# Kernel tuning notes

Measured on AMD Instinct MI355X. Metric: run time of the kernel, lower is better.

The kernel has to match this reference:

```python
import jax, jax.numpy as jnp
import numpy as np

N = 100000
E = 3200000
IN_DIM, HID, MLP_HID, K = 3, 64, 128, 15


def setup_inputs() -> dict:
    key = jax.random.key(0)
    ks = jax.random.split(key, 10)
    x = jax.random.normal(ks[0], (N, IN_DIM), dtype=jnp.float32)
    edge_index = jax.random.randint(ks[1], (2, E), 0, N, dtype=jnp.int32)
    def glorot(k, shape):
        lim = float(np.sqrt(6.0 / (shape[0] + shape[1])))
        return jax.random.uniform(k, shape, jnp.float32, -lim, lim)
    return {
        "x": x,
        "edge_index": edge_index,
        "W1": glorot(ks[2], (IN_DIM, HID)), "b1": jnp.zeros((HID,), jnp.float32),
        "W2": glorot(ks[3], (HID, HID)),    "b2": jnp.zeros((HID,), jnp.float32),
        "Wm1": glorot(ks[4], (HID, MLP_HID)), "bm1": jnp.zeros((MLP_HID,), jnp.float32),
        "Wm2": glorot(ks[5], (MLP_HID, K)),   "bm2": jnp.zeros((K,), jnp.float32),
    }


def _gcn_layer(h, W, b, src, dst, deg_inv_sqrt, n):
    # h: [N, Fin] -> [N, Fout]; GCNConv: D^-1/2 (A+I) D^-1/2 (h W) + b
    hw = h @ W  # dense GEMM first (Fin small)
    norm = deg_inv_sqrt[src] * deg_inv_sqrt[dst]  # [E+N]
    msg = hw[src] * norm[:, None]                 # irregular gather, [E+N, Fout]
    out = jax.ops.segment_sum(msg, dst, num_segments=n)  # scatter-add
    return out + b


def reference(x, edge_index, W1, b1, W2, b2, Wm1, bm1, Wm2, bm2):
    n = x.shape[0]
    loops = jnp.arange(n, dtype=edge_index.dtype)
    src = jnp.concatenate([edge_index[0], loops])  # self-loops appended
    dst = jnp.concatenate([edge_index[1], loops])
    deg = jax.ops.segment_sum(jnp.ones_like(dst, dtype=x.dtype), dst, num_segments=n)
    deg_inv_sqrt = jnp.where(deg > 0, jax.lax.rsqrt(jnp.maximum(deg, 1.0)), 0.0)

    h = jax.nn.elu(_gcn_layer(x, W1, b1, src, dst, deg_inv_sqrt, n))
    h = jax.nn.elu(_gcn_layer(h, W2, b2, src, dst, deg_inv_sqrt, n))
    # MLP (dropout is identity in eval mode)
    h = jax.nn.elu(h @ Wm1 + bm1)
    H = h @ Wm2 + bm2
    return jax.nn.softmax(H, axis=1)  # [N, K]
```

## Files before the change

kernel.cpp:

```cpp
#include <hip/hip_runtime.h>
#include <hip/hip_fp16.h>
#include <math.h>


#define SPAN 128
#define CAP  4608
#define CH   8192
#define EPT  32
#define H2P  88
#define MSP2 136

typedef _Float16 v8hf __attribute__((ext_vector_type(8)));
typedef float    v4f  __attribute__((ext_vector_type(4)));

__device__ __forceinline__ float elu(float v) { return v > 0.f ? v : expm1f(v); }

__global__ __launch_bounds__(256) void prep_kernel(const float* __restrict__ W2,
    const float* __restrict__ Wm1, __half* __restrict__ W2t, __half* __restrict__ Wm1t,
    int* __restrict__ cursor, int NBK) {
    int tid = blockIdx.x * 256 + threadIdx.x;
    if (tid < NBK) cursor[tid] = 0;
    if (tid < 64 * 64) {
        int f = tid >> 6, k = tid & 63;
        W2t[f * 64 + k] = __float2half(W2[k * 64 + f]);
    }
    if (tid < 128 * 64) {
        int j = tid >> 6, f = tid & 63;
        Wm1t[j * 64 + f] = __float2half(Wm1[f * 128 + j]);
    }
}

__global__ __launch_bounds__(256) void scatter_kernel(const int* __restrict__ src,
    const int* __restrict__ dst, int* __restrict__ cursor, unsigned* __restrict__ colb,
    int E, int NBK) {
    __shared__ int hist[1024];
    __shared__ unsigned gb[1024];
    int tid = threadIdx.x;
    int chunk = blockIdx.x;
    for (int i = tid; i < NBK; i += 256) hist[i] = 0;
    __syncthreads();
    int base = chunk * CH;
    int cnt = min(CH, E - base);
    unsigned br[EPT], dt[EPT];
#pragma unroll
    for (int j = 0; j < EPT; ++j) {
        int idx = j * 256 + tid;
        br[j] = 0xFFFFFFFFu;
        if (idx < cnt) {
            int e = base + idx;
            int s = src[e], d = dst[e];
            int b = d >> 7;
            int r = atomicAdd(&hist[b], 1);
            br[j] = ((unsigned)b << 13) | (unsigned)r;
            dt[j] = ((unsigned)(d & 127) << 17) | (unsigned)s;
        }
    }
    __syncthreads();
    for (int b = tid; b < NBK; b += 256) {
        int c = hist[b];
        gb[b] = (unsigned)(b * CAP) + (c ? (unsigned)atomicAdd(&cursor[b], c) : 0u);
    }
    __syncthreads();
#pragma unroll
    for (int j = 0; j < EPT; ++j) {
        if (br[j] != 0xFFFFFFFFu) {
            int b = br[j] >> 13;
            int r = br[j] & 8191;
            unsigned pos = gb[b] + (unsigned)r;
            if (pos < (unsigned)(b + 1) * CAP) colb[pos] = dt[j];
        }
    }
}

__global__ __launch_bounds__(256) void csr_sort_kernel(const unsigned* __restrict__ colb,
    const int* __restrict__ cursor, const float* __restrict__ x,
    int* __restrict__ row_ptr, int* __restrict__ col,
    float* __restrict__ dis, __half* __restrict__ sxh, int N, int NBK) {
    __shared__ unsigned ebuf[CAP];
    __shared__ int sbuf[CAP];
    __shared__ int cnt[SPAN], pref[SPAN], fill[SPAN];
    __shared__ int redbuf[256];
    int b = blockIdx.x, tid = threadIdx.x;
    int n = min(cursor[b], CAP);
    int base = b * CAP;
    int partial = 0;
    for (int i2 = tid; i2 < b; i2 += 256) partial += min(cursor[i2], CAP);
    redbuf[tid] = partial;
    if (tid < SPAN) cnt[tid] = 0;
    for (int i = tid; i < n; i += 256) ebuf[i] = colb[base + i];
    __syncthreads();
    for (int off = 128; off; off >>= 1) {
        if (tid < off) redbuf[tid] += redbuf[tid + off];
        __syncthreads();
    }
    int bb = redbuf[0];
    for (int i = tid; i < n; i += 256) atomicAdd(&cnt[(ebuf[i] >> 17) & 127], 1);
    __syncthreads();
    if (tid < SPAN) pref[tid] = cnt[tid];
    __syncthreads();
    for (int off = 1; off < SPAN; off <<= 1) {
        int xv = (tid < SPAN && tid >= off) ? pref[tid - off] : 0;
        __syncthreads();
        if (tid < SPAN) pref[tid] += xv;
        __syncthreads();
    }
    if (tid < SPAN) {
        int ex = pref[tid] - cnt[tid];
        fill[tid] = ex;
        int node = b * SPAN + tid;
        if (node < N) {
            row_ptr[node] = bb + ex;
            float r = rsqrtf((float)(cnt[tid] + 1));
            dis[node] = r;
            __half2 h0 = __floats2half2_rn(r * x[node * 3 + 0], r * x[node * 3 + 1]);
            __half2 h1 = __floats2half2_rn(r * x[node * 3 + 2], 0.f);
            uint2 w; w.x = *(unsigned*)&h0; w.y = *(unsigned*)&h1;
            *(uint2*)(sxh + (size_t)node * 4) = w;
        }
    }
    if (b == NBK - 1 && tid == 0) row_ptr[N] = bb + n;
    __syncthreads();
    for (int i = tid; i < n; i += 256) {
        unsigned e = ebuf[i];
        int pos = atomicAdd(&fill[(e >> 17) & 127], 1);
        sbuf[pos] = (int)(e & 0x1FFFF);
    }
    __syncthreads();
    for (int i = tid; i < n; i += 256) col[bb + i] = sbuf[i];
}

__global__ void agg3_kernel(const __half* __restrict__ sxh, const int* __restrict__ row_ptr,
                            const int* __restrict__ col, const float* __restrict__ dis,
                            const float* __restrict__ W1, const float* __restrict__ b1,
                            __half* __restrict__ s1h, int N) {
    int wave = (blockIdx.x * blockDim.x + threadIdx.x) >> 6;
    int lane = threadIdx.x & 63;
    if (wave >= N) return;
    int d = wave;
    int start = row_ptr[d], end = row_ptr[d + 1];
    float a0 = 0.f, a1 = 0.f, a2v = 0.f;
    for (int i = start + lane; i < end; i += 64) {
        uint2 rq = *(const uint2*)(sxh + (size_t)col[i] * 4);
        float2 u0 = __half22float2(*(__half2*)&rq.x);
        float2 u1 = __half22float2(*(__half2*)&rq.y);
        a0 += u0.x; a1 += u0.y; a2v += u1.x;
    }
#pragma unroll
    for (int off = 32; off; off >>= 1) {
        a0  += __shfl_xor(a0, off);
        a1  += __shfl_xor(a1, off);
        a2v += __shfl_xor(a2v, off);
    }
    {
        uint2 rq = *(const uint2*)(sxh + (size_t)d * 4);
        float2 u0 = __half22float2(*(__half2*)&rq.x);
        float2 u1 = __half22float2(*(__half2*)&rq.y);
        a0 += u0.x; a1 += u0.y; a2v += u1.x;
    }
    float r = dis[d];
    float v = r * (a0 * W1[lane] + a1 * W1[64 + lane] + a2v * W1[128 + lane]) + b1[lane];
    s1h[(size_t)d * 64 + lane] = __float2half(r * elu(v));
}

__global__ void agg64_kernel(const __half2* __restrict__ s1h, const int* __restrict__ row_ptr,
                             const int* __restrict__ col, const float* __restrict__ dis,
                             __half2* __restrict__ a2h, int N) {
    int wave = (blockIdx.x * blockDim.x + threadIdx.x) >> 6;
    int lane = threadIdx.x & 63;
    int hl = lane & 31;
    int d = wave * 2 + (lane >> 5);
    bool act = d < N;
    int start = 0, end = 0;
    if (act) { start = row_ptr[d]; end = row_ptr[d + 1]; }
    float a0x = 0.f, a0y = 0.f, a1x = 0.f, a1y = 0.f;
    float a2x = 0.f, a2y = 0.f, a3x = 0.f, a3y = 0.f;
    float a4x = 0.f, a4y = 0.f, a5x = 0.f, a5y = 0.f;
    float a6x = 0.f, a6y = 0.f, a7x = 0.f, a7y = 0.f;
    if (act) {
        float2 v = __half22float2(s1h[(size_t)d * 32 + hl]);
        a0x = v.x; a0y = v.y;
    }
    int i = start;
    for (; i + 7 < end; i += 8) {
        int c0 = col[i],     c1 = col[i + 1], c2 = col[i + 2], c3 = col[i + 3];
        int c4 = col[i + 4], c5 = col[i + 5], c6 = col[i + 6], c7 = col[i + 7];
        float2 v0 = __half22float2(s1h[(size_t)c0 * 32 + hl]);
        float2 v1 = __half22float2(s1h[(size_t)c1 * 32 + hl]);
        float2 v2 = __half22float2(s1h[(size_t)c2 * 32 + hl]);
        float2 v3 = __half22float2(s1h[(size_t)c3 * 32 + hl]);
        float2 v4 = __half22float2(s1h[(size_t)c4 * 32 + hl]);
        float2 v5 = __half22float2(s1h[(size_t)c5 * 32 + hl]);
        float2 v6 = __half22float2(s1h[(size_t)c6 * 32 + hl]);
        float2 v7 = __half22float2(s1h[(size_t)c7 * 32 + hl]);
        a0x += v0.x; a0y += v0.y; a1x += v1.x; a1y += v1.y;
        a2x += v2.x; a2y += v2.y; a3x += v3.x; a3y += v3.y;
        a4x += v4.x; a4y += v4.y; a5x += v5.x; a5y += v5.y;
        a6x += v6.x; a6y += v6.y; a7x += v7.x; a7y += v7.y;
    }
    for (; i < end; ++i) {
        float2 v = __half22float2(s1h[(size_t)col[i] * 32 + hl]);
        a0x += v.x; a0y += v.y;
    }
    if (act) {
        float r = dis[d];
        float ox = r * (((a0x + a1x) + (a2x + a3x)) + ((a4x + a5x) + (a6x + a7x)));
        float oy = r * (((a0y + a1y) + (a2y + a3y)) + ((a4y + a5y) + (a6y + a7y)));
        a2h[(size_t)d * 32 + hl] = __floats2half2_rn(ox, oy);
    }
}

__global__ __launch_bounds__(256) void h1_kernel(const __half* __restrict__ a2h,
    const __half* __restrict__ W2t, const float* __restrict__ b2g,
    const __half* __restrict__ Wm1t, const float* __restrict__ bm1g,
    const float* __restrict__ Wm2g, const float* __restrict__ bm2g,
    float* __restrict__ out, int N) {
    __shared__ __align__(16) __half h2s[64 * H2P];
    __shared__ __align__(16) __half ms[64 * MSP2];
    __shared__ float Wt2[128 * 16];
    __shared__ float b2s[64], bm1s[128], bm2s[16];
    int tid = threadIdx.x;
    if (tid < 64)  b2s[tid]  = b2g[tid];
    if (tid < 128) bm1s[tid] = bm1g[tid];
    if (tid < 16)  bm2s[tid] = (tid < 15) ? bm2g[tid] : 0.f;
    for (int i = tid; i < 128 * 16; i += 256) {
        int j = i >> 4, c = i & 15;
        Wt2[i] = (c < 15) ? Wm2g[j * 15 + c] : 0.f;
    }
    __syncthreads();

    int wave = tid >> 6, lane = tid & 63;
    int q = lane >> 4, l16 = lane & 15;
    int base = blockIdx.x * 64;

    {
        int nodeRow = base + wave * 16 + l16;
        size_t arow = (size_t)min(nodeRow, N - 1) * 64;
        v8hf af0 = *(const v8hf*)(a2h + arow + q * 8);
        v8hf af1 = *(const v8hf*)(a2h + arow + 32 + q * 8);
#pragma unroll
        for (int fb = 0; fb < 4; ++fb) {
            float bb = b2s[fb * 16 + l16];
            v4f acc = {bb, bb, bb, bb};
            v8hf b0 = *(const v8hf*)(W2t + (fb * 16 + l16) * 64 + q * 8);
            v8hf b1 = *(const v8hf*)(W2t + (fb * 16 + l16) * 64 + 32 + q * 8);
            acc = __builtin_amdgcn_mfma_f32_16x16x32_f16(af0, b0, acc, 0, 0, 0);
            acc = __builtin_amdgcn_mfma_f32_16x16x32_f16(af1, b1, acc, 0, 0, 0);
#pragma unroll
            for (int r = 0; r < 4; ++r)
                h2s[(wave * 16 + q * 4 + r) * H2P + fb * 16 + l16] =
                    __float2half(elu(acc[r]));
        }
    }
    __syncthreads();
    {
        int arow = (wave * 16 + l16) * H2P;
        v8hf af0 = *(const v8hf*)(h2s + arow + q * 8);
        v8hf af1 = *(const v8hf*)(h2s + arow + 32 + q * 8);
#pragma unroll
        for (int jb = 0; jb < 8; ++jb) {
            float bb = bm1s[jb * 16 + l16];
            v4f acc = {bb, bb, bb, bb};
            v8hf b0 = *(const v8hf*)(Wm1t + (jb * 16 + l16) * 64 + q * 8);
            v8hf b1 = *(const v8hf*)(Wm1t + (jb * 16 + l16) * 64 + 32 + q * 8);
            acc = __builtin_amdgcn_mfma_f32_16x16x32_f16(af0, b0, acc, 0, 0, 0);
            acc = __builtin_amdgcn_mfma_f32_16x16x32_f16(af1, b1, acc, 0, 0, 0);
#pragma unroll
            for (int r = 0; r < 4; ++r)
                ms[(wave * 16 + q * 4 + r) * MSP2 + jb * 16 + l16] =
                    __float2half(elu(acc[r]));
        }
    }
    __syncthreads();
    {
        int c = l16;
        int nloc = wave * 4 + q;
#pragma unroll
        for (int it = 0; it < 4; ++it) {
            int row = it * 16 + nloc;
            float acc = bm2s[c];
            const __half2* mrow = (const __half2*)(ms + row * MSP2);
#pragma unroll 4
            for (int j2 = 0; j2 < 64; ++j2) {
                float2 u = __half22float2(mrow[j2]);
                acc = fmaf(u.x, Wt2[(2 * j2) * 16 + c],
                      fmaf(u.y, Wt2[(2 * j2 + 1) * 16 + c], acc));
            }
            float lg = (c < 15) ? acc : -1e30f;
            float mx = lg;
            mx = fmaxf(mx, __shfl_xor(mx, 1));
            mx = fmaxf(mx, __shfl_xor(mx, 2));
            mx = fmaxf(mx, __shfl_xor(mx, 4));
            mx = fmaxf(mx, __shfl_xor(mx, 8));
            float ex = (c < 15) ? __expf(lg - mx) : 0.f;
            float sden = ex;
            sden += __shfl_xor(sden, 1);
            sden += __shfl_xor(sden, 2);
            sden += __shfl_xor(sden, 4);
            sden += __shfl_xor(sden, 8);
            int node = base + row;
            if (c < 15 && node < N)
                out[(size_t)node * 15 + c] = ex / sden;
        }
    }
}

extern "C" void kernel_launch(void* const* d_in, const int* in_sizes, int n_in,
                              void* d_out, int out_size, void* d_ws, size_t ws_size,
                              hipStream_t stream) {
    const float* x   = (const float*)d_in[0];
    const int*   ei  = (const int*)d_in[1];
    const float* W1  = (const float*)d_in[2];
    const float* b1  = (const float*)d_in[3];
    const float* W2  = (const float*)d_in[4];
    const float* b2  = (const float*)d_in[5];
    const float* Wm1 = (const float*)d_in[6];
    const float* bm1 = (const float*)d_in[7];
    const float* Wm2 = (const float*)d_in[8];
    const float* bm2 = (const float*)d_in[9];
    float* out = (float*)d_out;

    int N = in_sizes[0] / 3;
    int E = in_sizes[1] / 2;
    const int* src = ei;
    const int* dst = ei + E;
    int NBK = (N + SPAN - 1) / SPAN;

    uintptr_t p = (uintptr_t)d_ws;
    auto carve = [&](size_t bytes) -> void* {
        p = (p + 255) & ~(uintptr_t)255;
        void* r = (void*)p;
        p += bytes;
        return r;
    };
    __half*   a2h     = (__half*)carve((size_t)N * 64 * 2);
    __half*   s1h     = (__half*)carve((size_t)N * 64 * 2);
    int*      cursor  = (int*)carve((size_t)NBK * 4);
    int*      row_ptr = (int*)carve((size_t)(N + 1) * 4);
    float*    dis     = (float*)carve((size_t)N * 4);
    __half*   sxh     = (__half*)carve((size_t)N * 8);
    int*      col     = (int*)carve((size_t)E * 4);
    __half*   W2t     = (__half*)carve(64 * 64 * 2);
    __half*   Wm1t    = (__half*)carve(128 * 64 * 2);
    unsigned* colb = (unsigned*)a2h;

    int nChunks = (E + CH - 1) / CH;
    int waveBlocks3  = (N + 3) / 4;
    int waveBlocks64 = (N + 7) / 8;
    int nTiles = (N + 63) / 64;
    prep_kernel<<<32, 256, 0, stream>>>(W2, Wm1, W2t, Wm1t, cursor, NBK);
    scatter_kernel<<<nChunks, 256, 0, stream>>>(src, dst, cursor, colb, E, NBK);
    csr_sort_kernel<<<NBK, 256, 0, stream>>>(colb, cursor, x, row_ptr, col, dis, sxh, N, NBK);
    agg3_kernel<<<waveBlocks3, 256, 0, stream>>>(sxh, row_ptr, col, dis, W1, b1, s1h, N);
    agg64_kernel<<<waveBlocks64, 256, 0, stream>>>((const __half2*)s1h, row_ptr, col, dis,
                                                   (__half2*)a2h, N);
    h1_kernel<<<nTiles, 256, 0, stream>>>(a2h, W2t, b2, Wm1t, bm1, Wm2, bm2, out, N);
}
```

Baseline: 267.9 us.

## Move final MLP layer to MFMA and fold weight prep into scatter kernel

The final 128x15 projection in h1_kernel now runs on MFMA 16x16x32 f16 using a prepacked fp16 Wm2 fragment held in registers, replacing the scalar FMA loop over a shared-memory weight table. The block-level shared-memory staging of biases and Wm2, along with its barrier, is removed. The prep kernel is eliminated: cursor zeroing becomes a memset and the weight transposes run in an extra block of the scatter kernel, which now uses 512 threads with 16 edges per thread. This cuts a launch and the epilogue ALU work, but rounds Wm2 to fp16.

```diff
diff --git a/kernel.cpp b/kernel.cpp
--- a/kernel.cpp
+++ b/kernel.cpp
@@ -6,7 +6,7 @@
 #define SPAN 128
 #define CAP  4608
 #define CH   8192
-#define EPT  32
+#define EPT  16
 #define H2P  88
 #define MSP2 136
 
@@ -15,36 +15,41 @@
 
 __device__ __forceinline__ float elu(float v) { return v > 0.f ? v : expm1f(v); }
 
-__global__ __launch_bounds__(256) void prep_kernel(const float* __restrict__ W2,
-    const float* __restrict__ Wm1, __half* __restrict__ W2t, __half* __restrict__ Wm1t,
-    int* __restrict__ cursor, int NBK) {
-    int tid = blockIdx.x * 256 + threadIdx.x;
-    if (tid < NBK) cursor[tid] = 0;
-    if (tid < 64 * 64) {
-        int f = tid >> 6, k = tid & 63;
-        W2t[f * 64 + k] = __float2half(W2[k * 64 + f]);
-    }
-    if (tid < 128 * 64) {
-        int j = tid >> 6, f = tid & 63;
-        Wm1t[j * 64 + f] = __float2half(Wm1[f * 128 + j]);
-    }
-}
-
-__global__ __launch_bounds__(256) void scatter_kernel(const int* __restrict__ src,
+__global__ __launch_bounds__(512) void scatter_kernel(const int* __restrict__ src,
     const int* __restrict__ dst, int* __restrict__ cursor, unsigned* __restrict__ colb,
-    int E, int NBK) {
+    const float* __restrict__ W2, const float* __restrict__ Wm1,
+    const float* __restrict__ Wm2, __half* __restrict__ W2t,
+    __half* __restrict__ Wm1t, __half* __restrict__ Wm2p,
+    int E, int NBK, int nChunks) {
+    int tid = threadIdx.x;
+    if ((int)blockIdx.x == nChunks) {
+        for (int i = tid; i < 64 * 64; i += 512) {
+            int f = i >> 6, k = i & 63;
+            W2t[f * 64 + k] = __float2half(W2[k * 64 + f]);
+        }
+        for (int i = tid; i < 128 * 64; i += 512) {
+            int j = i >> 6, f = i & 63;
+            Wm1t[j * 64 + f] = __float2half(Wm1[f * 128 + j]);
+        }
+        for (int i = tid; i < 4 * 64 * 8; i += 512) {
+            int j = i & 7, l = (i >> 3) & 63, t = i >> 9;
+            int k = t * 32 + (l >> 4) * 8 + j;
+            int c = l & 15;
+            Wm2p[i] = (c < 15) ? __float2half(Wm2[k * 15 + c]) : __half(0.f);
+        }
+        return;
+    }
     __shared__ int hist[1024];
     __shared__ unsigned gb[1024];
-    int tid = threadIdx.x;
     int chunk = blockIdx.x;
-    for (int i = tid; i < NBK; i += 256) hist[i] = 0;
+    for (int i = tid; i < NBK; i += 512) hist[i] = 0;
     __syncthreads();
     int base = chunk * CH;
     int cnt = min(CH, E - base);
     unsigned br[EPT], dt[EPT];
 #pragma unroll
     for (int j = 0; j < EPT; ++j) {
-        int idx = j * 256 + tid;
+        int idx = j * 512 + tid;
         br[j] = 0xFFFFFFFFu;
         if (idx < cnt) {
             int e = base + idx;
@@ -56,7 +61,7 @@
         }
     }
     __syncthreads();
-    for (int b = tid; b < NBK; b += 256) {
+    for (int b = tid; b < NBK; b += 512) {
         int c = hist[b];
         gb[b] = (unsigned)(b * CAP) + (c ? (unsigned)atomicAdd(&cursor[b], c) : 0u);
     }
@@ -212,25 +217,20 @@
 __global__ __launch_bounds__(256) void h1_kernel(const __half* __restrict__ a2h,
     const __half* __restrict__ W2t, const float* __restrict__ b2g,
     const __half* __restrict__ Wm1t, const float* __restrict__ bm1g,
-    const float* __restrict__ Wm2g, const float* __restrict__ bm2g,
+    const __half* __restrict__ Wm2p, const float* __restrict__ bm2g,
     float* __restrict__ out, int N) {
     __shared__ __align__(16) __half h2s[64 * H2P];
     __shared__ __align__(16) __half ms[64 * MSP2];
-    __shared__ float Wt2[128 * 16];
-    __shared__ float b2s[64], bm1s[128], bm2s[16];
     int tid = threadIdx.x;
-    if (tid < 64)  b2s[tid]  = b2g[tid];
-    if (tid < 128) bm1s[tid] = bm1g[tid];
-    if (tid < 16)  bm2s[tid] = (tid < 15) ? bm2g[tid] : 0.f;
-    for (int i = tid; i < 128 * 16; i += 256) {
-        int j = i >> 4, c = i & 15;
-        Wt2[i] = (c < 15) ? Wm2g[j * 15 + c] : 0.f;
-    }
-    __syncthreads();
-
     int wave = tid >> 6, lane = tid & 63;
     int q = lane >> 4, l16 = lane & 15;
     int base = blockIdx.x * 64;
+
+    v8hf wc[4];
+#pragma unroll
+    for (int t = 0; t < 4; ++t)
+        wc[t] = *(const v8hf*)(Wm2p + ((size_t)(t * 64 + lane)) * 8);
+    float bbc = (l16 < 15) ? bm2g[l16] : 0.f;
 
     {
         int nodeRow = base + wave * 16 + l16;
@@ -239,7 +239,7 @@
         v8hf af1 = *(const v8hf*)(a2h + arow + 32 + q * 8);
 #pragma unroll
         for (int fb = 0; fb < 4; ++fb) {
-            float bb = b2s[fb * 16 + l16];
+            float bb = b2g[fb * 16 + l16];
             v4f acc = {bb, bb, bb, bb};
             v8hf b0 = *(const v8hf*)(W2t + (fb * 16 + l16) * 64 + q * 8);
             v8hf b1 = *(const v8hf*)(W2t + (fb * 16 + l16) * 64 + 32 + q * 8);
@@ -258,7 +258,7 @@
         v8hf af1 = *(const v8hf*)(h2s + arow + 32 + q * 8);
 #pragma unroll
         for (int jb = 0; jb < 8; ++jb) {
-            float bb = bm1s[jb * 16 + l16];
+            float bb = bm1g[jb * 16 + l16];
             v4f acc = {bb, bb, bb, bb};
             v8hf b0 = *(const v8hf*)(Wm1t + (jb * 16 + l16) * 64 + q * 8);
             v8hf b1 = *(const v8hf*)(Wm1t + (jb * 16 + l16) * 64 + 32 + q * 8);
@@ -272,34 +272,30 @@
     }
     __syncthreads();
     {
-        int c = l16;
-        int nloc = wave * 4 + q;
-#pragma unroll
-        for (int it = 0; it < 4; ++it) {
-            int row = it * 16 + nloc;
-            float acc = bm2s[c];
-            const __half2* mrow = (const __half2*)(ms + row * MSP2);
-#pragma unroll 4
-            for (int j2 = 0; j2 < 64; ++j2) {
-                float2 u = __half22float2(mrow[j2]);
-                acc = fmaf(u.x, Wt2[(2 * j2) * 16 + c],
-                      fmaf(u.y, Wt2[(2 * j2 + 1) * 16 + c], acc));
-            }
-            float lg = (c < 15) ? acc : -1e30f;
+        int arow = (wave * 16 + l16) * MSP2;
+        v4f accC = {bbc, bbc, bbc, bbc};
+#pragma unroll
+        for (int t = 0; t < 4; ++t) {
+            v8hf a = *(const v8hf*)(ms + arow + t * 32 + q * 8);
+            accC = __builtin_amdgcn_mfma_f32_16x16x32_f16(a, wc[t], accC, 0, 0, 0);
+        }
+#pragma unroll
+        for (int r = 0; r < 4; ++r) {
+            float lg = (l16 < 15) ? accC[r] : -1e30f;
             float mx = lg;
             mx = fmaxf(mx, __shfl_xor(mx, 1));
             mx = fmaxf(mx, __shfl_xor(mx, 2));
             mx = fmaxf(mx, __shfl_xor(mx, 4));
             mx = fmaxf(mx, __shfl_xor(mx, 8));
-            float ex = (c < 15) ? __expf(lg - mx) : 0.f;
+            float ex = (l16 < 15) ? __expf(lg - mx) : 0.f;
             float sden = ex;
             sden += __shfl_xor(sden, 1);
             sden += __shfl_xor(sden, 2);
             sden += __shfl_xor(sden, 4);
             sden += __shfl_xor(sden, 8);
-            int node = base + row;
-            if (c < 15 && node < N)
-                out[(size_t)node * 15 + c] = ex / sden;
+            int node = base + wave * 16 + q * 4 + r;
+            if (l16 < 15 && node < N)
+                out[(size_t)node * 15 + l16] = ex / sden;
         }
     }
 }
@@ -341,17 +337,20 @@
     int*      col     = (int*)carve((size_t)E * 4);
     __half*   W2t     = (__half*)carve(64 * 64 * 2);
     __half*   Wm1t    = (__half*)carve(128 * 64 * 2);
+    __half*   Wm2p    = (__half*)carve(4 * 64 * 8 * 2);
     unsigned* colb = (unsigned*)a2h;
 
     int nChunks = (E + CH - 1) / CH;
     int waveBlocks3  = (N + 3) / 4;
     int waveBlocks64 = (N + 7) / 8;
     int nTiles = (N + 63) / 64;
-    prep_kernel<<<32, 256, 0, stream>>>(W2, Wm1, W2t, Wm1t, cursor, NBK);
-    scatter_kernel<<<nChunks, 256, 0, stream>>>(src, dst, cursor, colb, E, NBK);
+
+    hipMemsetAsync(cursor, 0, (size_t)NBK * 4, stream);
+    scatter_kernel<<<nChunks + 1, 512, 0, stream>>>(src, dst, cursor, colb,
+        W2, Wm1, Wm2, W2t, Wm1t, Wm2p, E, NBK, nChunks);
     csr_sort_kernel<<<NBK, 256, 0, stream>>>(colb, cursor, x, row_ptr, col, dis, sxh, N, NBK);
     agg3_kernel<<<waveBlocks3, 256, 0, stream>>>(sxh, row_ptr, col, dis, W1, b1, s1h, N);
     agg64_kernel<<<waveBlocks64, 256, 0, stream>>>((const __half2*)s1h, row_ptr, col, dis,
                                                    (__half2*)a2h, N);
-    h1_kernel<<<nTiles, 256, 0, stream>>>(a2h, W2t, b2, Wm1t, bm1, Wm2, bm2, out, N);
-}
+    h1_kernel<<<nTiles, 256, 0, stream>>>(a2h, W2t, b2, Wm1t, bm1, Wm2p, bm2, out, N);
+}
```

After: 246.7 us. -7.9%, faster.
